# Kernel optimization log

Hardware: AMD Instinct MI355X
Metric: run time of the kernel (lower is better)

Reference implementation:

```python
import jax, jax.numpy as jnp
import numpy as np

EMBED_DIM = 4096
N_HEADS = 16
HEAD_DIM = 256
ROTARY_DIM = 64
SCALE_ATTN = 16.0  # sqrt(head_dim)
MASK_VAL = -65504.0


def setup_inputs() -> dict:
    key = jax.random.key(0)
    ks = jax.random.split(key, 5)
    B, S, D = 2, 2048, EMBED_DIM
    sc = 1.0 / np.sqrt(D)
    return {
        "hidden_states": jax.random.normal(ks[0], (B, S, D), dtype=jnp.float32),
        "Wq": jax.random.normal(ks[1], (D, D), dtype=jnp.float32) * sc,
        "Wk": jax.random.normal(ks[2], (D, D), dtype=jnp.float32) * sc,
        "Wv": jax.random.normal(ks[3], (D, D), dtype=jnp.float32) * sc,
        "Wo": jax.random.normal(ks[4], (D, D), dtype=jnp.float32) * sc,
        "position_ids": jnp.arange(S, dtype=jnp.int32),
    }


def _gptj_rope(x, position_ids):
    # x: [B, S, H, rotary_dim]; GPT-J interleaved (rotate_every_two) RoPE
    half = ROTARY_DIM // 2
    inv_freq = 1.0 / (10000.0 ** (jnp.arange(0, ROTARY_DIM, 2, dtype=jnp.float32) / ROTARY_DIM))
    sinusoid = position_ids.astype(jnp.float32)[:, None] * inv_freq[None, :]  # [S, half]
    sin = jnp.repeat(jnp.sin(sinusoid), 2, axis=-1)[None, :, None, :]  # [1,S,1,rot]
    cos = jnp.repeat(jnp.cos(sinusoid), 2, axis=-1)[None, :, None, :]
    x1 = x[..., 0::2]
    x2 = x[..., 1::2]
    rotated = jnp.stack([-x2, x1], axis=-1).reshape(x.shape)
    return x * cos + rotated * sin


def reference(hidden_states, Wq, Wk, Wv, Wo, position_ids):
    B, S, D = hidden_states.shape
    H, hd, rot = N_HEADS, HEAD_DIM, ROTARY_DIM

    q = (hidden_states @ Wq.T).reshape(B, S, H, hd)
    k = (hidden_states @ Wk.T).reshape(B, S, H, hd)
    v = (hidden_states @ Wv.T).reshape(B, S, H, hd)

    # rotary on first rotary_dim dims only
    q = jnp.concatenate([_gptj_rope(q[..., :rot], position_ids), q[..., rot:]], axis=-1)
    k = jnp.concatenate([_gptj_rope(k[..., :rot], position_ids), k[..., rot:]], axis=-1)

    q = q.transpose(0, 2, 1, 3)  # [B,H,S,hd]
    k = k.transpose(0, 2, 1, 3)
    v = v.transpose(0, 2, 1, 3)

    scores = jnp.einsum("bhqd,bhkd->bhqk", q, k)
    causal = jnp.tril(jnp.ones((S, S), dtype=bool))[None, None]
    # faithful to source: mask with -65504 BEFORE dividing by scale_attn
    scores = jnp.where(causal, scores, MASK_VAL) / SCALE_ATTN
    probs = jax.nn.softmax(scores, axis=-1)
    ctx = jnp.einsum("bhqk,bhkd->bhqd", probs, v)  # [B,H,S,hd]

    ctx = ctx.transpose(0, 2, 1, 3).reshape(B, S, D)
    return ctx @ Wo.T
```

## Files before the change

kernel.cpp:

```cpp
#include <hip/hip_runtime.h>
#include <stdint.h>

typedef unsigned short u16;
typedef short short8 __attribute__((ext_vector_type(8)));
typedef __bf16 bf16x8 __attribute__((ext_vector_type(8)));
typedef float f32x4 __attribute__((ext_vector_type(4)));

__device__ __forceinline__ u16 f2bf(float f) {
  uint32_t u = __float_as_uint(f);
  u += 0x7fffu + ((u >> 16) & 1u);
  return (u16)(u >> 16);
}
__device__ __forceinline__ float bf2f(u16 h) {
  return __uint_as_float(((uint32_t)h) << 16);
}
__device__ __forceinline__ f32x4 mfma16(short8 a, short8 b, f32x4 c) {
  return __builtin_amdgcn_mfma_f32_16x16x32_bf16(
      __builtin_bit_cast(bf16x8, a), __builtin_bit_cast(bf16x8, b), c, 0, 0, 0);
}
__device__ __forceinline__ uint32_t cvtpk_bf16(float lo, float hi) {
  uint32_t r;
  asm("v_cvt_pk_bf16_f32 %0, %1, %2" : "=v"(r) : "v"(lo), "v"(hi));
  return r;
}
__device__ __forceinline__ void gld_lds16(const u16* g, u16* lds_base) {
  __builtin_amdgcn_global_load_lds(
      (__attribute__((address_space(1))) void*)g,
      (__attribute__((address_space(3))) void*)lds_base, 16, 0, 0);
}
#define BAR() do { asm volatile("" ::: "memory"); \
                   __builtin_amdgcn_s_barrier(); \
                   asm volatile("" ::: "memory"); } while (0)

__global__ __launch_bounds__(256) void cvt_bf16(const float* __restrict__ s,
                                                u16* __restrict__ d) {
  int i = blockIdx.x * 256 + threadIdx.x;
  const float4* s4 = (const float4*)s;
  float4 a = s4[2 * i], b = s4[2 * i + 1];
  uint4 o;
  o.x = (uint32_t)f2bf(a.x) | ((uint32_t)f2bf(a.y) << 16);
  o.y = (uint32_t)f2bf(a.z) | ((uint32_t)f2bf(a.w) << 16);
  o.z = (uint32_t)f2bf(b.x) | ((uint32_t)f2bf(b.y) << 16);
  o.w = (uint32_t)f2bf(b.z) | ((uint32_t)f2bf(b.w) << 16);
  ((uint4*)d)[i] = o;
}

template <int MODE>
__global__ __launch_bounds__(512, 2) void gemm_nt(const u16* __restrict__ A,
                                                  const u16* __restrict__ W,
                                                  void* __restrict__ outp,
                                                  float oscale) {
  constexpr int Kd = 4096;
  __shared__ __align__(16) u16 As[2][2][8192];
  __shared__ __align__(16) u16 Bs[2][2][8192];
  const int tid = threadIdx.x;
  const int wid = tid >> 6, l = tid & 63;
  const int lg = (l >> 4) & 3, lc = l & 15;
  const int wm = wid >> 2, wn = wid & 3;
  const int bid0 = blockIdx.x;
  const int bid = (bid0 & 7) * 32 + (bid0 >> 3);
  const int m0 = (bid >> 4) * 256, n0 = (bid & 15) * 256;

  const int srow = tid >> 3;
  const int scol = ((tid & 7) ^ (srow & 7)) * 8;
  const int arow = m0 + srow;
  const int browb = n0 + ((srow >> 5) & 1) * 64 + (srow & 31);

#define STAGE_A(BUF, H, T) do { \
    const u16* g0 = A + (size_t)(arow + (H) * 64) * Kd + (T) * 64 + scol; \
    gld_lds16(g0, &As[BUF][H][wid * 512]); \
    gld_lds16(g0 + (size_t)128 * Kd, &As[BUF][H][4096 + wid * 512]); \
  } while (0)
#define STAGE_B(BUF, H, T) do { \
    const u16* g0 = W + (size_t)(browb + (H) * 32) * Kd + (T) * 64 + scol; \
    gld_lds16(g0, &Bs[BUF][H][wid * 512]); \
    gld_lds16(g0 + (size_t)128 * Kd, &Bs[BUF][H][4096 + wid * 512]); \
  } while (0)

  f32x4 acc[8][4];
#pragma unroll
  for (int i = 0; i < 8; ++i)
#pragma unroll
    for (int j = 0; j < 4; ++j) acc[i][j] = (f32x4)0.0f;

  const int axor = (lc & 7);

  short8 af[4][2], b0f[2][2], b1f[2][2];

#define LDA(MQ) do { \
    const char* Ab_ = (const char*)As[buf][MQ] + (wm * 64 + lc) * 128; \
    _Pragma("unroll") for (int f = 0; f < 4; ++f) \
      _Pragma("unroll") for (int kk = 0; kk < 2; ++kk) \
        af[f][kk] = *(const short8*)(Ab_ + f * 2048 + (((kk * 4 + lg) ^ axor) << 4)); \
  } while (0)
#define LDB(DST, NQ) do { \
    const char* Bb_ = (const char*)Bs[buf][NQ] + (wn * 32 + lc) * 128; \
    _Pragma("unroll") for (int g = 0; g < 2; ++g) \
      _Pragma("unroll") for (int kk = 0; kk < 2; ++kk) \
        DST[g][kk] = *(const short8*)(Bb_ + g * 2048 + (((kk * 4 + lg) ^ axor) << 4)); \
  } while (0)
#define MM(MQ, NQ, BF) do { \
    __builtin_amdgcn_s_setprio(1); \
    _Pragma("unroll") for (int f = 0; f < 4; ++f) \
      _Pragma("unroll") for (int g = 0; g < 2; ++g) \
        _Pragma("unroll") for (int kk = 0; kk < 2; ++kk) \
          acc[(MQ) * 4 + f][(NQ) * 2 + g] = \
              mfma16(af[f][kk], BF[g][kk], acc[(MQ) * 4 + f][(NQ) * 2 + g]); \
    __builtin_amdgcn_s_setprio(0); \
  } while (0)

  STAGE_A(0, 0, 0); STAGE_B(0, 1, 0); STAGE_B(0, 0, 0); STAGE_A(0, 1, 0);
  STAGE_A(1, 0, 1); STAGE_B(1, 1, 1);
  asm volatile("s_waitcnt vmcnt(4)" ::: "memory");
  BAR();

#pragma unroll 1
  for (int t = 0; t < 62; ++t) {
    const int buf = t & 1, nbuf = buf ^ 1;
    LDA(0); LDB(b0f, 0); LDB(b1f, 1);
    STAGE_B(nbuf, 0, t + 1); STAGE_A(nbuf, 1, t + 1);
    BAR(); MM(0, 0, b0f); MM(0, 1, b1f); BAR();
    LDA(1);
    STAGE_A(buf, 0, t + 2); STAGE_B(buf, 1, t + 2);
    asm volatile("s_waitcnt vmcnt(4)" ::: "memory");
    BAR(); MM(1, 1, b1f); MM(1, 0, b0f); BAR();
  }
  {
    const int buf = 0, nbuf = 1;
    LDA(0); LDB(b0f, 0); LDB(b1f, 1);
    STAGE_B(nbuf, 0, 63); STAGE_A(nbuf, 1, 63);
    BAR(); MM(0, 0, b0f); MM(0, 1, b1f); BAR();
    LDA(1);
    asm volatile("s_waitcnt vmcnt(0)" ::: "memory");
    BAR(); MM(1, 1, b1f); MM(1, 0, b0f); BAR();
  }
  {
    const int buf = 1;
    LDA(0); LDB(b0f, 0); LDB(b1f, 1);
    BAR(); MM(0, 0, b0f); MM(0, 1, b1f); BAR();
    LDA(1);
    BAR(); MM(1, 1, b1f); MM(1, 0, b0f); BAR();
  }
#undef MM
#undef LDB
#undef LDA
#undef STAGE_A
#undef STAGE_B

  const int gr0 = m0 + wm * 128, gc0 = n0 + wn * 64;
#pragma unroll
  for (int mf = 0; mf < 8; ++mf)
#pragma unroll
    for (int nf = 0; nf < 4; ++nf)
#pragma unroll
      for (int r = 0; r < 4; ++r) {
        float v = acc[mf][nf][r] * oscale;
        int gr = gr0 + mf * 16 + lg * 4 + r;
        int gc = gc0 + nf * 16 + lc;
        if constexpr (MODE == 0) {
          ((u16*)outp)[((size_t)(((gr >> 11) * 16 + (gc >> 8)) * 2048 +
                                 (gr & 2047))) * 256 + (gc & 255)] = f2bf(v);
        } else if constexpr (MODE == 1) {
          ((u16*)outp)[(size_t)((gr >> 11) * 4096 + gc) * 2048 + (gr & 2047)] =
              f2bf(v);
        } else {
          ((float*)outp)[(size_t)gr * 4096 + gc] = v;
        }
      }
}

__global__ __launch_bounds__(256) void rope_qk(u16* __restrict__ Qb,
                                               u16* __restrict__ Kb,
                                               const int* __restrict__ pos) {
  int idx = blockIdx.x * 256 + threadIdx.x;
  int pair = idx & 31;
  int s = (idx >> 5) & 2047;
  int bh = (idx >> 16) & 31;
  u16* T = (idx >> 21) ? Kb : Qb;
  float p = (float)pos[s];
  float inv = powf(10000.0f, -(float)pair * (1.0f / 32.0f));
  float ang = p * inv, sn, cs;
  sincosf(ang, &sn, &cs);
  u16* base = T + ((size_t)bh * 2048 + s) * 256 + pair * 2;
  float x1 = bf2f(base[0]), x2 = bf2f(base[1]);
  base[0] = f2bf(x1 * cs - x2 * sn);
  base[1] = f2bf(x2 * cs + x1 * sn);
}

__global__ __launch_bounds__(256) void flash_attn(const u16* __restrict__ Q,
                                                  const u16* __restrict__ K,
                                                  const u16* __restrict__ Vt,
                                                  u16* __restrict__ ctx) {
  __shared__ u16 Ks[2][32 * 256];
  __shared__ u16 Vs[2][256 * 32];
  __shared__ u16 P[4][16 * 40];

  const int bid = blockIdx.x;
  const int bidp = (bid & 7) * 128 + (bid >> 3);
  const int bh = bidp >> 5;
  const int qi = bidp & 31;
  const int q0 = 1984 - qi * 64;
  const int tid = threadIdx.x;
  const int wid = tid >> 6, l = tid & 63;
  const int lg = l >> 4, lc = l & 15;
  const int qr = q0 + wid * 16;

  const u16* Qh = Q + (size_t)bh * 2048 * 256;
  const u16* Kh = K + (size_t)bh * 2048 * 256;
  const u16* Vh = Vt + (size_t)bh * 256 * 2048;

  int krow[4], kcol[4], vrow[4], vcol[4];
#pragma unroll
  for (int jj = 0; jj < 4; ++jj) {
    int j = wid * 4 + jj;
    krow[jj] = 2 * j + (l >> 5);
    kcol[jj] = ((((l & 31) << 4) ^ ((krow[jj] & 7) << 4)) >> 1);
    vrow[jj] = j * 16 + (l >> 2);
    vcol[jj] = ((((l & 3) << 4) ^ (((vrow[jj] >> 1) & 3) << 4)) >> 1);
  }

  short8 qf[8];
#pragma unroll
  for (int kk = 0; kk < 8; ++kk)
    qf[kk] = *(const short8*)&Qh[(size_t)(qr + lc) * 256 + kk * 32 + lg * 8];

  f32x4 o[16];
#pragma unroll
  for (int nf = 0; nf < 16; ++nf) o[nf] = (f32x4)0.0f;
  float mrow = -1e30f;
  float lrow = 0.0f;

  uint32_t* Pw = (uint32_t*)P[wid];
  const u16* Pm = P[wid];

  const int ntiles = q0 / 32 + 2;

#pragma unroll
  for (int jj = 0; jj < 4; ++jj) {
    gld_lds16(Kh + (size_t)krow[jj] * 256 + kcol[jj], &Ks[0][(wid * 4 + jj) * 512]);
    gld_lds16(Vh + (size_t)vrow[jj] * 2048 + vcol[jj], &Vs[0][(wid * 4 + jj) * 512]);
  }
  __syncthreads();

  for (int t = 0; t < ntiles; ++t) {
    const int buf = t & 1;
    if (t + 1 < ntiles) {
      const int kv1 = (t + 1) << 5;
#pragma unroll
      for (int jj = 0; jj < 4; ++jj) {
        gld_lds16(Kh + (size_t)(kv1 + krow[jj]) * 256 + kcol[jj],
                  &Ks[buf ^ 1][(wid * 4 + jj) * 512]);
        gld_lds16(Vh + (size_t)vrow[jj] * 2048 + kv1 + vcol[jj],
                  &Vs[buf ^ 1][(wid * 4 + jj) * 512]);
      }
    }
    const int kv0 = t << 5;
    const char* KsB = (const char*)Ks[buf];
    const char* VsB = (const char*)Vs[buf];

    f32x4 s0 = (f32x4)0.0f, s1 = (f32x4)0.0f;
#pragma unroll
    for (int kk = 0; kk < 8; ++kk) {
      const int cb = kk * 64 + lg * 16;
      short8 k0 = *(const short8*)(KsB + lc * 512 + (cb ^ ((lc & 7) << 4)));
      short8 k1 = *(const short8*)(KsB + (16 + lc) * 512 + (cb ^ ((lc & 7) << 4)));
      s0 = mfma16(k0, qf[kk], s0);
      s1 = mfma16(k1, qf[kk], s1);
    }
    float sv[8];
#pragma unroll
    for (int r = 0; r < 4; ++r) { sv[r] = s0[r]; sv[4 + r] = s1[r]; }
    if (kv0 + 31 > qr) {
#pragma unroll
      for (int f = 0; f < 2; ++f)
#pragma unroll
        for (int r = 0; r < 4; ++r) {
          int kvg = kv0 + f * 16 + lg * 4 + r;
          if (kvg > qr + lc) sv[f * 4 + r] = -1e30f;
        }
    }
    float m8 = fmaxf(fmaxf(fmaxf(sv[0], sv[1]), fmaxf(sv[2], sv[3])),
                     fmaxf(fmaxf(sv[4], sv[5]), fmaxf(sv[6], sv[7])));
    float pm = fmaxf(m8, __shfl_xor(m8, 16));
    pm = fmaxf(pm, __shfl_xor(pm, 32));
    if (__ballot(pm > mrow)) {
      float mn = fmaxf(mrow, pm);
      float alpha = __builtin_amdgcn_exp2f(mrow - mn);
      lrow *= alpha;
      float aa[4];
#pragma unroll
      for (int r = 0; r < 4; ++r) aa[r] = __shfl(alpha, lg * 4 + r);
#pragma unroll
      for (int nf = 0; nf < 16; ++nf) {
        f32x4 t4 = o[nf];
#pragma unroll
        for (int r = 0; r < 4; ++r) t4[r] *= aa[r];
        o[nf] = t4;
      }
      mrow = mn;
    }
    float p[8];
#pragma unroll
    for (int j = 0; j < 8; ++j) p[j] = __builtin_amdgcn_exp2f(sv[j] - mrow);
    float ps = ((p[0] + p[1]) + (p[2] + p[3])) + ((p[4] + p[5]) + (p[6] + p[7]));
    ps += __shfl_xor(ps, 16);
    ps += __shfl_xor(ps, 32);
    lrow += ps;
    asm volatile("" ::: "memory");
    Pw[lc * 20 + lg * 2 + 0] = cvtpk_bf16(p[0], p[1]);
    Pw[lc * 20 + lg * 2 + 1] = cvtpk_bf16(p[2], p[3]);
    Pw[lc * 20 + 8 + lg * 2 + 0] = cvtpk_bf16(p[4], p[5]);
    Pw[lc * 20 + 8 + lg * 2 + 1] = cvtpk_bf16(p[6], p[7]);
    asm volatile("" ::: "memory");
    short8 pf = *(const short8*)&Pm[lc * 40 + lg * 8];
#pragma unroll
    for (int nf = 0; nf < 16; ++nf) {
      const int d = nf * 16 + lc;
      short8 vf = *(const short8*)(VsB + d * 64 + ((lg * 16) ^ (((d >> 1) & 3) << 4)));
      o[nf] = mfma16(pf, vf, o[nf]);
    }
    asm volatile("" ::: "memory");
    __syncthreads();
  }

  float il = 1.0f / lrow;
  float ia[4];
#pragma unroll
  for (int r = 0; r < 4; ++r) ia[r] = __shfl(il, lg * 4 + r);
  const int crow0 = (bh >> 4) * 2048 + qr;
  const int ccol0 = (bh & 15) * 256;
#pragma unroll
  for (int nf = 0; nf < 16; ++nf)
#pragma unroll
    for (int r = 0; r < 4; ++r)
      ctx[(size_t)(crow0 + lg * 4 + r) * 4096 + ccol0 + nf * 16 + lc] =
          f2bf(o[nf][r] * ia[r]);
}

extern "C" void kernel_launch(void* const* d_in, const int* in_sizes, int n_in,
                              void* d_out, int out_size, void* d_ws, size_t ws_size,
                              hipStream_t stream) {
  const float* hidden = (const float*)d_in[0];
  const float* Wq = (const float*)d_in[1];
  const float* Wk = (const float*)d_in[2];
  const float* Wv = (const float*)d_in[3];
  const float* Wo = (const float*)d_in[4];
  const int* pos = (const int*)d_in[5];

  const size_t NEL = 16777216;
  if (ws_size < 6 * NEL * sizeof(u16)) return;

  u16* hb = (u16*)d_ws;
  u16* wq = hb + NEL;
  u16* wk = wq + NEL;
  u16* wv = wk + NEL;
  u16* wo = wv + NEL;
  u16* vt = wo + NEL;
  u16* ctx = hb;
  u16* qb = (u16*)d_out;
  u16* kb = qb + NEL;

  cvt_bf16<<<8192, 256, 0, stream>>>(hidden, hb);
  cvt_bf16<<<8192, 256, 0, stream>>>(Wq, wq);
  cvt_bf16<<<8192, 256, 0, stream>>>(Wk, wk);
  cvt_bf16<<<8192, 256, 0, stream>>>(Wv, wv);
  cvt_bf16<<<8192, 256, 0, stream>>>(Wo, wo);

  gemm_nt<0><<<256, 512, 0, stream>>>(hb, wq, qb, 0.09016844f);
  gemm_nt<0><<<256, 512, 0, stream>>>(hb, wk, kb, 1.0f);
  gemm_nt<1><<<256, 512, 0, stream>>>(hb, wv, vt, 1.0f);

  rope_qk<<<16384, 256, 0, stream>>>(qb, kb, pos);

  flash_attn<<<1024, 256, 0, stream>>>(qb, kb, vt, ctx);

  gemm_nt<2><<<256, 512, 0, stream>>>(ctx, wo, d_out, 1.0f);
}
```

Measured before the change: 747.4 us.

## Merge bf16 conversions into one launch and tune flash attention softmax loop

```diff
diff --git a/kernel.cpp b/kernel.cpp
--- a/kernel.cpp
+++ b/kernel.cpp
@@ -32,11 +32,19 @@
                    __builtin_amdgcn_s_barrier(); \
                    asm volatile("" ::: "memory"); } while (0)
 
-__global__ __launch_bounds__(256) void cvt_bf16(const float* __restrict__ s,
-                                                u16* __restrict__ d) {
-  int i = blockIdx.x * 256 + threadIdx.x;
-  const float4* s4 = (const float4*)s;
-  float4 a = s4[2 * i], b = s4[2 * i + 1];
+__global__ __launch_bounds__(256) void cvt_bf16_5(const float* __restrict__ s0,
+                                                  const float* __restrict__ s1,
+                                                  const float* __restrict__ s2,
+                                                  const float* __restrict__ s3,
+                                                  const float* __restrict__ s4,
+                                                  u16* __restrict__ dbase) {
+  const int gb = blockIdx.x;
+  const int t = gb >> 13;
+  const float* s = t == 0 ? s0 : t == 1 ? s1 : t == 2 ? s2 : t == 3 ? s3 : s4;
+  u16* d = dbase + (size_t)t * 16777216;
+  int i = (gb & 8191) * 256 + threadIdx.x;
+  const float4* s4p = (const float4*)s;
+  float4 a = s4p[2 * i], b = s4p[2 * i + 1];
   uint4 o;
   o.x = (uint32_t)f2bf(a.x) | ((uint32_t)f2bf(a.y) << 16);
   o.y = (uint32_t)f2bf(a.z) | ((uint32_t)f2bf(a.w) << 16);
@@ -178,7 +186,7 @@
   int bh = (idx >> 16) & 31;
   u16* T = (idx >> 21) ? Kb : Qb;
   float p = (float)pos[s];
-  float inv = powf(10000.0f, -(float)pair * (1.0f / 32.0f));
+  float inv = __builtin_amdgcn_exp2f((float)pair * -0.41524101186407984f);
   float ang = p * inv, sn, cs;
   sincosf(ang, &sn, &cs);
   u16* base = T + ((size_t)bh * 2048 + s) * 256 + pair * 2;
@@ -259,6 +267,7 @@
     const char* VsB = (const char*)Vs[buf];
 
     f32x4 s0 = (f32x4)0.0f, s1 = (f32x4)0.0f;
+    __builtin_amdgcn_s_setprio(1);
 #pragma unroll
     for (int kk = 0; kk < 8; ++kk) {
       const int cb = kk * 64 + lg * 16;
@@ -267,6 +276,15 @@
       s0 = mfma16(k0, qf[kk], s0);
       s1 = mfma16(k1, qf[kk], s1);
     }
+    __builtin_amdgcn_s_setprio(0);
+
+    short8 vfr[16];
+#pragma unroll
+    for (int nf = 0; nf < 16; ++nf) {
+      const int d = nf * 16 + lc;
+      vfr[nf] = *(const short8*)(VsB + d * 64 + ((lg * 16) ^ (((d >> 1) & 3) << 4)));
+    }
+
     float sv[8];
 #pragma unroll
     for (int r = 0; r < 4; ++r) { sv[r] = s0[r]; sv[4 + r] = s1[r]; }
@@ -283,8 +301,8 @@
                      fmaxf(fmaxf(sv[4], sv[5]), fmaxf(sv[6], sv[7])));
     float pm = fmaxf(m8, __shfl_xor(m8, 16));
     pm = fmaxf(pm, __shfl_xor(pm, 32));
-    if (__ballot(pm > mrow)) {
-      float mn = fmaxf(mrow, pm);
+    if (__ballot(pm > mrow + 8.0f)) {
+      float mn = (pm > mrow + 8.0f) ? pm : mrow;
       float alpha = __builtin_amdgcn_exp2f(mrow - mn);
       lrow *= alpha;
       float aa[4];
@@ -302,10 +320,7 @@
     float p[8];
 #pragma unroll
     for (int j = 0; j < 8; ++j) p[j] = __builtin_amdgcn_exp2f(sv[j] - mrow);
-    float ps = ((p[0] + p[1]) + (p[2] + p[3])) + ((p[4] + p[5]) + (p[6] + p[7]));
-    ps += __shfl_xor(ps, 16);
-    ps += __shfl_xor(ps, 32);
-    lrow += ps;
+    lrow += ((p[0] + p[1]) + (p[2] + p[3])) + ((p[4] + p[5]) + (p[6] + p[7]));
     asm volatile("" ::: "memory");
     Pw[lc * 20 + lg * 2 + 0] = cvtpk_bf16(p[0], p[1]);
     Pw[lc * 20 + lg * 2 + 1] = cvtpk_bf16(p[2], p[3]);
@@ -313,17 +328,17 @@
     Pw[lc * 20 + 8 + lg * 2 + 1] = cvtpk_bf16(p[6], p[7]);
     asm volatile("" ::: "memory");
     short8 pf = *(const short8*)&Pm[lc * 40 + lg * 8];
-#pragma unroll
-    for (int nf = 0; nf < 16; ++nf) {
-      const int d = nf * 16 + lc;
-      short8 vf = *(const short8*)(VsB + d * 64 + ((lg * 16) ^ (((d >> 1) & 3) << 4)));
-      o[nf] = mfma16(pf, vf, o[nf]);
-    }
+    __builtin_amdgcn_s_setprio(1);
+#pragma unroll
+    for (int nf = 0; nf < 16; ++nf) o[nf] = mfma16(pf, vfr[nf], o[nf]);
+    __builtin_amdgcn_s_setprio(0);
     asm volatile("" ::: "memory");
     __syncthreads();
   }
 
-  float il = 1.0f / lrow;
+  float lt = lrow + __shfl_xor(lrow, 16);
+  lt += __shfl_xor(lt, 32);
+  float il = 1.0f / lt;
   float ia[4];
 #pragma unroll
   for (int r = 0; r < 4; ++r) ia[r] = __shfl(il, lg * 4 + r);
@@ -360,11 +375,7 @@
   u16* qb = (u16*)d_out;
   u16* kb = qb + NEL;
 
-  cvt_bf16<<<8192, 256, 0, stream>>>(hidden, hb);
-  cvt_bf16<<<8192, 256, 0, stream>>>(Wq, wq);
-  cvt_bf16<<<8192, 256, 0, stream>>>(Wk, wk);
-  cvt_bf16<<<8192, 256, 0, stream>>>(Wv, wv);
-  cvt_bf16<<<8192, 256, 0, stream>>>(Wo, wo);
+  cvt_bf16_5<<<40960, 256, 0, stream>>>(hidden, Wq, Wk, Wv, Wo, hb);
 
   gemm_nt<0><<<256, 512, 0, stream>>>(hb, wq, qb, 0.09016844f);
   gemm_nt<0><<<256, 512, 0, stream>>>(hb, wk, kb, 1.0f);
```

Measured after the change: 738.6 us. No clear change (-1.2%).
